# Optimization experiments

Measured on AMD Instinct MI355X. Metric: run time of the kernel, lower is better.

Reference implementation:

```python
import jax, jax.numpy as jnp
import numpy as np

N = 100000      # nodes
E = 3200000     # edges (avg degree 32)
IN = 128        # in_channels
H = 32          # hidden dim
OUT = 64        # out_channels
L = 31          # number of SGConv layers


def setup_inputs() -> dict:
    key = jax.random.key(0)
    ks = jax.random.split(key, 10)
    x = jax.random.normal(ks[0], (N, IN), dtype=jnp.float32)
    edge_index = jax.random.randint(ks[1], (2, E), 0, N, dtype=jnp.int32)
    s = 0.05
    W1 = jax.random.normal(ks[2], (H, IN), dtype=jnp.float32) * s
    b1 = jnp.zeros((H,), dtype=jnp.float32)
    Wc = jax.random.normal(ks[3], (L, H, H), dtype=jnp.float32) * s
    bc = jnp.zeros((L, H), dtype=jnp.float32)
    W32 = jax.random.normal(ks[4], (OUT, 32 * H), dtype=jnp.float32) * s
    b32 = jnp.zeros((OUT,), dtype=jnp.float32)
    return {"x": x, "edge_index": edge_index, "W1": W1, "b1": b1,
            "Wc": Wc, "bc": bc, "W32": W32, "b32": b32}


def mynorm(t):
    # min/max over feature axis (dim=1 of [N, C]; last axis in general)
    mn = jnp.min(t, axis=-1, keepdims=True)
    mx = jnp.max(t, axis=-1, keepdims=True)
    return 2.0 * (t - mn) / (mx - mn + 1e-8) - 1.0


def reference(x, edge_index, W1, b1, Wc, bc, W32, b32):
    n = x.shape[0]
    loops = jnp.arange(n, dtype=edge_index.dtype)
    row = jnp.concatenate([edge_index[0], loops])  # source
    col = jnp.concatenate([edge_index[1], loops])  # target
    # symmetric GCN normalization (PyG gcn_norm, add_self_loops=True)
    deg = jax.ops.segment_sum(jnp.ones_like(row, dtype=x.dtype), col, num_segments=n)
    dis = jnp.where(deg > 0, jax.lax.rsqrt(deg), 0.0)
    nrm = (dis[row] * dis[col])[:, None]  # [E+N, 1]

    def prop(h):
        # out[col] += norm * h[row]
        return jax.ops.segment_sum(h[row] * nrm, col, num_segments=n)

    x0 = mynorm(jax.nn.relu(x @ W1.T + b1))  # [N, 32]

    def step(h, p):
        W, b = p
        y = prop(h) @ W.T + b  # SGConv K=1: propagate then linear
        return y, y

    _, ys = jax.lax.scan(step, x0, (Wc, bc))  # [31, N, 32]
    xs = jnp.concatenate([x0[None], ys], axis=0)  # [32, N, 32]
    m = mynorm(xs)
    # xx1 = x1; xxk = mynorm(xk) - mynorm(x_{k-2}); original uses raw x16 at slot 16
    feats = [x0, xs[1]]
    for k in range(2, 32):
        feats.append(xs[k] if k == 16 else m[k] - m[k - 2])
    cat = jnp.concatenate(feats, axis=1)  # [N, 1024]
    return cat @ W32.T + b32  # [N, 64]
```

## Files before the change

### kernel.cpp

```cpp
#include <hip/hip_runtime.h>
#include <hip/hip_fp16.h>

#define NN 100000
#define NE 3200000
#define NB8 12500
#define CAP 80

__global__ __launch_bounds__(256) void k_scatter(const int* __restrict__ ei, int* __restrict__ cursor,
                                                 int* __restrict__ csr_row, int p) {
    int e = blockIdx.x * 256 + threadIdx.x;
    if (e < NE) {
        int c = ei[NE + e];
        int lo = p * NB8;
        if (c >= lo && c < lo + NB8) {
            int pos = c * CAP + atomicAdd(&cursor[c], 1);
            csr_row[pos] = ei[e];
        }
    }
}

__global__ __launch_bounds__(256) void k_dis(const int* __restrict__ cursor, float* __restrict__ dis) {
    int i = blockIdx.x * 256 + threadIdx.x;
    if (i < NN) dis[i] = 1.0f / sqrtf((float)(cursor[i] + 1));
}

__global__ __launch_bounds__(256) void k_x0(const float* __restrict__ x, const float* __restrict__ W1,
                                            const float* __restrict__ b1, const float* __restrict__ W32,
                                            const float* __restrict__ b32, const float* __restrict__ dis,
                                            __half* __restrict__ h0, __half* __restrict__ ring0,
                                            float* __restrict__ out, float* __restrict__ Mhat,
                                            float* __restrict__ SCar) {
    __shared__ float sW1[32 * 128];
    __shared__ float sW32[64 * 32];
    __shared__ float sb1[32], sb32[64];
    int t = threadIdx.x;
    if (blockIdx.x == 0 && t == 0) SCar[0] = 1.0f;
    for (int i = t; i < 4096; i += 256) sW1[i] = W1[i];
    for (int i = t; i < 2048; i += 256) sW32[i] = W32[(i >> 5) * 1024 + (i & 31)];
    if (t < 32) sb1[t] = b1[t];
    if (t < 64) sb32[t] = b32[t];
    __syncthreads();
    int node = blockIdx.x * 256 + t;
    if (node >= NN) return;

    float acc[32];
#pragma unroll
    for (int c = 0; c < 32; c++) acc[c] = sb1[c];
    const float4* xr4 = (const float4*)(x + (long)node * 128);
    for (int q = 0; q < 32; q++) {
        float4 xv = xr4[q];
#pragma unroll
        for (int c = 0; c < 32; c++) {
            acc[c] += xv.x * sW1[c * 128 + q * 4] + xv.y * sW1[c * 128 + q * 4 + 1] +
                      xv.z * sW1[c * 128 + q * 4 + 2] + xv.w * sW1[c * 128 + q * 4 + 3];
        }
    }
    float mn = 1e30f, mx = -1e30f;
#pragma unroll
    for (int c = 0; c < 32; c++) {
        acc[c] = fmaxf(acc[c], 0.f);
        mn = fminf(mn, acc[c]);
        mx = fmaxf(mx, acc[c]);
    }
    float inv = 2.f / (mx - mn + 1e-8f);
#pragma unroll
    for (int c = 0; c < 32; c++) acc[c] = inv * (acc[c] - mn) - 1.f;
    float sc = dis[node];
    __half2* hr = (__half2*)(h0 + (long)node * 32);
#pragma unroll
    for (int q = 0; q < 16; q++) hr[q] = __floats2half2_rn(sc * acc[2 * q], sc * acc[2 * q + 1]);
    if (t == 0 && (blockIdx.x & 15) == 0) atomicMax((int*)&Mhat[0], __float_as_int(sc));
    float mn2 = 1e30f, mx2 = -1e30f;
#pragma unroll
    for (int c = 0; c < 32; c++) {
        mn2 = fminf(mn2, acc[c]);
        mx2 = fmaxf(mx2, acc[c]);
    }
    float inv2 = 2.f / (mx2 - mn2 + 1e-8f);
    __half2* rr = (__half2*)(ring0 + (long)node * 32);
#pragma unroll
    for (int q = 0; q < 16; q++)
        rr[q] = __floats2half2_rn(inv2 * (acc[2 * q] - mn2) - 1.f, inv2 * (acc[2 * q + 1] - mn2) - 1.f);
    float* orow = out + (long)node * 64;
    for (int o = 0; o < 64; o++) {
        float a = sb32[o];
#pragma unroll
        for (int j = 0; j < 32; j++) a += sW32[o * 32 + j] * acc[j];
        orow[o] = a;
    }
}

__global__ __launch_bounds__(256, 3) void k_layer(const __half* __restrict__ hin, __half* __restrict__ hout,
                                                  __half* __restrict__ ring, const float* __restrict__ dis,
                                                  const int* __restrict__ cnt, const int* __restrict__ csr_row,
                                                  const float* __restrict__ Wck, const float* __restrict__ bck,
                                                  const float* __restrict__ W32k, float* __restrict__ out,
                                                  float* __restrict__ Mhat, float* __restrict__ SCar, int k,
                                                  int rawfeat) {
    __shared__ float sWc[32 * 33];
    __shared__ float sW[64 * 33];
    __shared__ float sbc[32];
    int t = threadIdx.x;
    float SCin = SCar[k - 1];
    float SCk = SCin * fmaxf(Mhat[k - 1], 1e-30f);
    if (t == 0) SCar[k] = SCk;
    float invSCk = 1.0f / SCk;
    for (int i = t; i < 1024; i += 256) sWc[(i >> 5) * 33 + (i & 31)] = Wck[i];
    for (int i = t; i < 2048; i += 256) sW[(i >> 5) * 33 + (i & 31)] = W32k[(i >> 5) * 1024 + (i & 31)];
    if (t < 32) sbc[t] = bck[t];
    __syncthreads();

    int wave = t >> 6, lane = t & 63;
    int sub = lane >> 3, q = lane & 7;
    int node = blockIdx.x * 32 + wave * 8 + sub;
    int sl = sub * 8;

    const uint2* __restrict__ h2 = (const uint2*)hin;
    int e0 = node * CAP;
    int e1 = e0 + cnt[node];
    float di = dis[node];

    float a0, a1, a2, a3, b0 = 0.f, b1 = 0.f, b2 = 0.f, b3 = 0.f;
    {
        uint2 u = h2[(long)node * 8 + q];
        float2 lo = __half22float2(*(__half2*)&u.x);
        float2 hi = __half22float2(*(__half2*)&u.y);
        a0 = lo.x; a1 = lo.y; a2 = hi.x; a3 = hi.y;
    }
    int base = e0;
    while (base + 8 <= e1) {
        int r = csr_row[base + q];
#pragma unroll
        for (int j = 0; j < 8; j += 2) {
            int r0 = __shfl(r, sl + j, 64);
            int r1 = __shfl(r, sl + j + 1, 64);
            uint2 u0 = h2[(long)r0 * 8 + q];
            uint2 u1 = h2[(long)r1 * 8 + q];
            float2 lo0 = __half22float2(*(__half2*)&u0.x), hi0 = __half22float2(*(__half2*)&u0.y);
            float2 lo1 = __half22float2(*(__half2*)&u1.x), hi1 = __half22float2(*(__half2*)&u1.y);
            a0 += lo0.x; a1 += lo0.y; a2 += hi0.x; a3 += hi0.y;
            b0 += lo1.x; b1 += lo1.y; b2 += hi1.x; b3 += hi1.y;
        }
        base += 8;
    }
    int rem = e1 - base;
    if (rem > 0) {
        int r = (q < rem) ? csr_row[base + q] : 0;
        for (int j = 0; j < rem; j++) {
            int rj = __shfl(r, sl + j, 64);
            uint2 u = h2[(long)rj * 8 + q];
            float2 lo = __half22float2(*(__half2*)&u.x), hi = __half22float2(*(__half2*)&u.y);
            a0 += lo.x; a1 += lo.y; a2 += hi.x; a3 += hi.y;
        }
    }
    float g0 = di * (a0 + b0), g1 = di * (a1 + b1), g2 = di * (a2 + b2), g3 = di * (a3 + b3);

    const float* wr0 = &sWc[(4 * q + 0) * 33];
    const float* wr1 = &sWc[(4 * q + 1) * 33];
    const float* wr2 = &sWc[(4 * q + 2) * 33];
    const float* wr3 = &sWc[(4 * q + 3) * 33];
    float y0 = 0.f, y1 = 0.f, y2 = 0.f, y3 = 0.f;
#pragma unroll
    for (int s = 0; s < 8; s++) {
        float t0 = __shfl(g0, sl + s, 64);
        float t1 = __shfl(g1, sl + s, 64);
        float t2 = __shfl(g2, sl + s, 64);
        float t3 = __shfl(g3, sl + s, 64);
        int jb = 4 * s;
        y0 += wr0[jb] * t0 + wr0[jb + 1] * t1 + wr0[jb + 2] * t2 + wr0[jb + 3] * t3;
        y1 += wr1[jb] * t0 + wr1[jb + 1] * t1 + wr1[jb + 2] * t2 + wr1[jb + 3] * t3;
        y2 += wr2[jb] * t0 + wr2[jb + 1] * t1 + wr2[jb + 2] * t2 + wr2[jb + 3] * t3;
        y3 += wr3[jb] * t0 + wr3[jb + 1] * t1 + wr3[jb + 2] * t2 + wr3[jb + 3] * t3;
    }
    y0 = SCin * y0 + sbc[4 * q + 0];
    y1 = SCin * y1 + sbc[4 * q + 1];
    y2 = SCin * y2 + sbc[4 * q + 2];
    y3 = SCin * y3 + sbc[4 * q + 3];

    {
        __half2 p0 = __floats2half2_rn(di * y0 * invSCk, di * y1 * invSCk);
        __half2 p1 = __floats2half2_rn(di * y2 * invSCk, di * y3 * invSCk);
        uint2 pw;
        pw.x = *(unsigned int*)&p0;
        pw.y = *(unsigned int*)&p1;
        ((uint2*)hout)[(long)node * 8 + q] = pw;
    }

    float mn = fminf(fminf(y0, y1), fminf(y2, y3));
    float mx = fmaxf(fmaxf(y0, y1), fmaxf(y2, y3));
#pragma unroll
    for (int m = 1; m < 8; m <<= 1) {
        mn = fminf(mn, __shfl_xor(mn, m, 64));
        mx = fmaxf(mx, __shfl_xor(mx, m, 64));
    }
    float inv = 2.f / (mx - mn + 1e-8f);
    float mv0 = inv * (y0 - mn) - 1.f, mv1 = inv * (y1 - mn) - 1.f;
    float mv2 = inv * (y2 - mn) - 1.f, mv3 = inv * (y3 - mn) - 1.f;

    if ((blockIdx.x & 15) == 0 && q == 0) {
        float rowmax = fmaxf(fabsf(mn), fabsf(mx));
        atomicMax((int*)&Mhat[k], __float_as_int(di * rowmax * invSCk));
    }

    float f0, f1, f2, f3;
    if (rawfeat) {
        f0 = y0; f1 = y1; f2 = y2; f3 = y3;
    } else {
        uint2 rv = ((const uint2*)ring)[(long)node * 8 + q];
        float2 rlo = __half22float2(*(__half2*)&rv.x);
        float2 rhi = __half22float2(*(__half2*)&rv.y);
        f0 = mv0 - rlo.x; f1 = mv1 - rlo.y; f2 = mv2 - rhi.x; f3 = mv3 - rhi.y;
    }
    {
        __half2 p0 = __floats2half2_rn(mv0, mv1);
        __half2 p1 = __floats2half2_rn(mv2, mv3);
        uint2 pw;
        pw.x = *(unsigned int*)&p0;
        pw.y = *(unsigned int*)&p1;
        ((uint2*)ring)[(long)node * 8 + q] = pw;
    }

    float o0 = 0.f, o1 = 0.f, o2 = 0.f, o3 = 0.f, o4 = 0.f, o5 = 0.f, o6 = 0.f, o7 = 0.f;
#pragma unroll
    for (int s = 0; s < 8; s++) {
        float t0 = __shfl(f0, sl + s, 64);
        float t1 = __shfl(f1, sl + s, 64);
        float t2 = __shfl(f2, sl + s, 64);
        float t3 = __shfl(f3, sl + s, 64);
        int jb = 4 * s;
        const float* w = &sW[(8 * q) * 33 + jb];
        o0 += w[0] * t0 + w[1] * t1 + w[2] * t2 + w[3] * t3; w += 33;
        o1 += w[0] * t0 + w[1] * t1 + w[2] * t2 + w[3] * t3; w += 33;
        o2 += w[0] * t0 + w[1] * t1 + w[2] * t2 + w[3] * t3; w += 33;
        o3 += w[0] * t0 + w[1] * t1 + w[2] * t2 + w[3] * t3; w += 33;
        o4 += w[0] * t0 + w[1] * t1 + w[2] * t2 + w[3] * t3; w += 33;
        o5 += w[0] * t0 + w[1] * t1 + w[2] * t2 + w[3] * t3; w += 33;
        o6 += w[0] * t0 + w[1] * t1 + w[2] * t2 + w[3] * t3; w += 33;
        o7 += w[0] * t0 + w[1] * t1 + w[2] * t2 + w[3] * t3;
    }
    float4* op = (float4*)(out + (long)node * 64 + 8 * q);
    float4 v0 = op[0], v1 = op[1];
    v0.x += o0; v0.y += o1; v0.z += o2; v0.w += o3;
    v1.x += o4; v1.y += o5; v1.z += o6; v1.w += o7;
    op[0] = v0;
    op[1] = v1;
}

extern "C" void kernel_launch(void* const* d_in, const int* in_sizes, int n_in, void* d_out, int out_size,
                              void* d_ws, size_t ws_size, hipStream_t stream) {
    const float* x = (const float*)d_in[0];
    const int* ei = (const int*)d_in[1];
    const float* W1 = (const float*)d_in[2];
    const float* b1 = (const float*)d_in[3];
    const float* Wc = (const float*)d_in[4];
    const float* bc = (const float*)d_in[5];
    const float* W32 = (const float*)d_in[6];
    const float* b32 = (const float*)d_in[7];
    float* out = (float*)d_out;

    uintptr_t base = ((uintptr_t)d_ws + 255) & ~(uintptr_t)255;
    __half* h0 = (__half*)base;
    __half* h1 = h0 + (long)NN * 32;
    __half* ring = h1 + (long)NN * 32;
    int* csr_row = (int*)(ring + (long)2 * NN * 32);
    int* cursor = csr_row + (long)NN * CAP;
    float* Mhat = (float*)(cursor + NN);
    float* SCar = Mhat + 64;
    float* dis = SCar + 64;

    hipMemsetAsync(cursor, 0, (NN + 128) * sizeof(int), stream);
    for (int p = 0; p < 8; p++)
        k_scatter<<<(NE + 255) / 256, 256, 0, stream>>>(ei, cursor, csr_row, p);
    k_dis<<<(NN + 255) / 256, 256, 0, stream>>>(cursor, dis);
    int NB = (NN + 255) / 256;
    k_x0<<<NB, 256, 0, stream>>>(x, W1, b1, W32, b32, dis, h0, ring, out, Mhat, SCar);

    for (int k = 1; k <= 31; k++) {
        const __half* hin = (k & 1) ? h0 : h1;
        __half* hout = (k & 1) ? h1 : h0;
        __half* ringk = ring + (long)(k & 1) * NN * 32;
        int raw = (k == 1 || k == 16) ? 1 : 0;
        k_layer<<<3125, 256, 0, stream>>>(hin, hout, ringk, dis, cursor, csr_row, Wc + (k - 1) * 1024,
                                          bc + (k - 1) * 32, W32 + 32 * k, out, Mhat, SCar, k, raw);
    }
}
```

Measured before the change: 2.319 ms.

## Split x0 projection across 8 lanes per node and drop the dis kernel

```diff
diff --git a/kernel.cpp b/kernel.cpp
--- a/kernel.cpp
+++ b/kernel.cpp
@@ -19,56 +19,64 @@
     }
 }
 
-__global__ __launch_bounds__(256) void k_dis(const int* __restrict__ cursor, float* __restrict__ dis) {
-    int i = blockIdx.x * 256 + threadIdx.x;
-    if (i < NN) dis[i] = 1.0f / sqrtf((float)(cursor[i] + 1));
-}
-
 __global__ __launch_bounds__(256) void k_x0(const float* __restrict__ x, const float* __restrict__ W1,
                                             const float* __restrict__ b1, const float* __restrict__ W32,
-                                            const float* __restrict__ b32, const float* __restrict__ dis,
+                                            const float* __restrict__ b32, const int* __restrict__ cnt,
                                             __half* __restrict__ h0, __half* __restrict__ ring0,
                                             float* __restrict__ out, float* __restrict__ Mhat,
                                             float* __restrict__ SCar) {
-    __shared__ float sW1[32 * 128];
-    __shared__ float sW32[64 * 32];
+    __shared__ float sW1[32 * 132];
+    __shared__ float sW32[64 * 33];
     __shared__ float sb1[32], sb32[64];
     int t = threadIdx.x;
     if (blockIdx.x == 0 && t == 0) SCar[0] = 1.0f;
-    for (int i = t; i < 4096; i += 256) sW1[i] = W1[i];
-    for (int i = t; i < 2048; i += 256) sW32[i] = W32[(i >> 5) * 1024 + (i & 31)];
+    for (int i = t; i < 4096; i += 256) sW1[(i >> 7) * 132 + (i & 127)] = W1[i];
+    for (int i = t; i < 2048; i += 256) sW32[(i >> 5) * 33 + (i & 31)] = W32[(i >> 5) * 1024 + (i & 31)];
     if (t < 32) sb1[t] = b1[t];
     if (t < 64) sb32[t] = b32[t];
     __syncthreads();
-    int node = blockIdx.x * 256 + t;
-    if (node >= NN) return;
+
+    int wave = t >> 6, lane = t & 63;
+    int sub = lane >> 3, q = lane & 7;
+    int node = blockIdx.x * 32 + wave * 8 + sub;
+
+    const float4* xr = (const float4*)(x + (long)node * 128 + q * 16);
+    float4 xv0 = xr[0], xv1 = xr[1], xv2 = xr[2], xv3 = xr[3];
 
     float acc[32];
 #pragma unroll
-    for (int c = 0; c < 32; c++) acc[c] = sb1[c];
-    const float4* xr4 = (const float4*)(x + (long)node * 128);
-    for (int q = 0; q < 32; q++) {
-        float4 xv = xr4[q];
-#pragma unroll
-        for (int c = 0; c < 32; c++) {
-            acc[c] += xv.x * sW1[c * 128 + q * 4] + xv.y * sW1[c * 128 + q * 4 + 1] +
-                      xv.z * sW1[c * 128 + q * 4 + 2] + xv.w * sW1[c * 128 + q * 4 + 3];
-        }
+    for (int c = 0; c < 32; c++) {
+        const float* w = &sW1[c * 132 + q * 16];
+        acc[c] = xv0.x * w[0] + xv0.y * w[1] + xv0.z * w[2] + xv0.w * w[3] +
+                 xv1.x * w[4] + xv1.y * w[5] + xv1.z * w[6] + xv1.w * w[7] +
+                 xv2.x * w[8] + xv2.y * w[9] + xv2.z * w[10] + xv2.w * w[11] +
+                 xv3.x * w[12] + xv3.y * w[13] + xv3.z * w[14] + xv3.w * w[15];
+    }
+#pragma unroll
+    for (int m = 1; m < 8; m <<= 1) {
+#pragma unroll
+        for (int c = 0; c < 32; c++) acc[c] += __shfl_xor(acc[c], m, 64);
     }
     float mn = 1e30f, mx = -1e30f;
 #pragma unroll
     for (int c = 0; c < 32; c++) {
-        acc[c] = fmaxf(acc[c], 0.f);
+        acc[c] = fmaxf(acc[c] + sb1[c], 0.f);
         mn = fminf(mn, acc[c]);
         mx = fmaxf(mx, acc[c]);
     }
     float inv = 2.f / (mx - mn + 1e-8f);
 #pragma unroll
     for (int c = 0; c < 32; c++) acc[c] = inv * (acc[c] - mn) - 1.f;
-    float sc = dis[node];
-    __half2* hr = (__half2*)(h0 + (long)node * 32);
-#pragma unroll
-    for (int q = 0; q < 16; q++) hr[q] = __floats2half2_rn(sc * acc[2 * q], sc * acc[2 * q + 1]);
+
+    float sc = 1.0f / sqrtf((float)(cnt[node] + 1));
+    {
+        __half2 p0 = __floats2half2_rn(sc * acc[4 * q], sc * acc[4 * q + 1]);
+        __half2 p1 = __floats2half2_rn(sc * acc[4 * q + 2], sc * acc[4 * q + 3]);
+        uint2 pw;
+        pw.x = *(unsigned int*)&p0;
+        pw.y = *(unsigned int*)&p1;
+        ((uint2*)h0)[(long)node * 8 + q] = pw;
+    }
     if (t == 0 && (blockIdx.x & 15) == 0) atomicMax((int*)&Mhat[0], __float_as_int(sc));
     float mn2 = 1e30f, mx2 = -1e30f;
 #pragma unroll
@@ -77,22 +85,31 @@
         mx2 = fmaxf(mx2, acc[c]);
     }
     float inv2 = 2.f / (mx2 - mn2 + 1e-8f);
-    __half2* rr = (__half2*)(ring0 + (long)node * 32);
-#pragma unroll
-    for (int q = 0; q < 16; q++)
-        rr[q] = __floats2half2_rn(inv2 * (acc[2 * q] - mn2) - 1.f, inv2 * (acc[2 * q + 1] - mn2) - 1.f);
-    float* orow = out + (long)node * 64;
-    for (int o = 0; o < 64; o++) {
-        float a = sb32[o];
-#pragma unroll
-        for (int j = 0; j < 32; j++) a += sW32[o * 32 + j] * acc[j];
-        orow[o] = a;
-    }
+    {
+        __half2 p0 = __floats2half2_rn(inv2 * (acc[4 * q] - mn2) - 1.f, inv2 * (acc[4 * q + 1] - mn2) - 1.f);
+        __half2 p1 = __floats2half2_rn(inv2 * (acc[4 * q + 2] - mn2) - 1.f, inv2 * (acc[4 * q + 3] - mn2) - 1.f);
+        uint2 pw;
+        pw.x = *(unsigned int*)&p0;
+        pw.y = *(unsigned int*)&p1;
+        ((uint2*)ring0)[(long)node * 8 + q] = pw;
+    }
+    float o[8];
+#pragma unroll
+    for (int i = 0; i < 8; i++) {
+        const float* w = &sW32[(8 * q + i) * 33];
+        float a = sb32[8 * q + i];
+#pragma unroll
+        for (int j = 0; j < 32; j++) a += w[j] * acc[j];
+        o[i] = a;
+    }
+    float4* op = (float4*)(out + (long)node * 64 + 8 * q);
+    op[0] = make_float4(o[0], o[1], o[2], o[3]);
+    op[1] = make_float4(o[4], o[5], o[6], o[7]);
 }
 
 __global__ __launch_bounds__(256, 3) void k_layer(const __half* __restrict__ hin, __half* __restrict__ hout,
-                                                  __half* __restrict__ ring, const float* __restrict__ dis,
-                                                  const int* __restrict__ cnt, const int* __restrict__ csr_row,
+                                                  __half* __restrict__ ring, const int* __restrict__ cnt,
+                                                  const int* __restrict__ csr_row,
                                                   const float* __restrict__ Wck, const float* __restrict__ bck,
                                                   const float* __restrict__ W32k, float* __restrict__ out,
                                                   float* __restrict__ Mhat, float* __restrict__ SCar, int k,
@@ -117,8 +134,9 @@
 
     const uint2* __restrict__ h2 = (const uint2*)hin;
     int e0 = node * CAP;
-    int e1 = e0 + cnt[node];
-    float di = dis[node];
+    int deg = cnt[node];
+    int e1 = e0 + deg;
+    float di = 1.0f / sqrtf((float)(deg + 1));
 
     float a0, a1, a2, a3, b0 = 0.f, b1 = 0.f, b2 = 0.f, b3 = 0.f;
     {
@@ -266,21 +284,18 @@
     int* cursor = csr_row + (long)NN * CAP;
     float* Mhat = (float*)(cursor + NN);
     float* SCar = Mhat + 64;
-    float* dis = SCar + 64;
 
     hipMemsetAsync(cursor, 0, (NN + 128) * sizeof(int), stream);
     for (int p = 0; p < 8; p++)
         k_scatter<<<(NE + 255) / 256, 256, 0, stream>>>(ei, cursor, csr_row, p);
-    k_dis<<<(NN + 255) / 256, 256, 0, stream>>>(cursor, dis);
-    int NB = (NN + 255) / 256;
-    k_x0<<<NB, 256, 0, stream>>>(x, W1, b1, W32, b32, dis, h0, ring, out, Mhat, SCar);
+    k_x0<<<3125, 256, 0, stream>>>(x, W1, b1, W32, b32, cursor, h0, ring, out, Mhat, SCar);
 
     for (int k = 1; k <= 31; k++) {
         const __half* hin = (k & 1) ? h0 : h1;
         __half* hout = (k & 1) ? h1 : h0;
         __half* ringk = ring + (long)(k & 1) * NN * 32;
         int raw = (k == 1 || k == 16) ? 1 : 0;
-        k_layer<<<3125, 256, 0, stream>>>(hin, hout, ringk, dis, cursor, csr_row, Wc + (k - 1) * 1024,
+        k_layer<<<3125, 256, 0, stream>>>(hin, hout, ringk, cursor, csr_row, Wc + (k - 1) * 1024,
                                           bc + (k - 1) * 32, W32 + 32 * k, out, Mhat, SCar, k, raw);
     }
 }
```

Result: no change. 2.315 ms (-0.2%).
